# Optimization experiments

Measured on AMD Instinct MI355X. Metric: run time of the kernel, lower is better.

## Reference

```python
import jax, jax.numpy as jnp
import numpy as np

N_NODES = 100000
N_EDGES = 3200000
NUM_FEATURES = 256
NUM_CLASSES = 1000


def gcn_conv(x, edge_index, W, b):
    # PyG GCNConv: h = XW; add self-loops; out = D^{-1/2} (A+I) D^{-1/2} h + b
    n = x.shape[0]
    h = x @ W  # [N, out]
    loop = jnp.arange(n)
    src = jnp.concatenate([edge_index[0], loop])
    dst = jnp.concatenate([edge_index[1], loop])
    ones = jnp.ones(src.shape[0], dtype=x.dtype)
    deg = jax.ops.segment_sum(ones, dst, num_segments=n)  # in-degree incl. self-loop
    dinv = jax.lax.rsqrt(deg)  # deg >= 1 because of self-loops
    norm = dinv[src] * dinv[dst]  # [E+N]
    out = jax.ops.segment_sum(h[src] * norm[:, None], dst, num_segments=n)
    return out + b


def setup_inputs() -> dict:
    key = jax.random.key(0)
    ks = jax.random.split(key, 12)
    x = jax.random.normal(ks[0], (N_NODES, NUM_FEATURES), dtype=jnp.float32)
    edge_index = jax.random.randint(ks[1], (2, N_EDGES), 0, N_NODES, dtype=jnp.int64)
    def glorot(k, shape):
        fan_in, fan_out = shape[0], shape[-1]
        lim = np.sqrt(6.0 / (fan_in + fan_out)).astype(np.float32)
        return jax.random.uniform(k, shape, jnp.float32, -lim, lim)
    W1 = glorot(ks[2], (NUM_FEATURES, 16)); b1 = jnp.zeros((16,), jnp.float32)
    W2 = glorot(ks[3], (16, 32));           b2 = jnp.zeros((32,), jnp.float32)
    conv_w = jax.random.normal(ks[4], (64, 32, 1, 3), jnp.float32) * 0.05  # OIHW
    conv_b = jnp.zeros((64,), jnp.float32)
    fc_w = jax.random.normal(ks[5], (NUM_CLASSES, 64), jnp.float32) * 0.05
    fc_b = jnp.zeros((NUM_CLASSES,), jnp.float32)
    return {"x": x, "edge_index": edge_index, "W1": W1, "b1": b1,
            "W2": W2, "b2": b2, "conv_w": conv_w, "conv_b": conv_b,
            "fc_w": fc_w, "fc_b": fc_b}


def reference(x, edge_index, W1, b1, W2, b2, conv_w, conv_b, fc_w, fc_b):
    h = jax.nn.relu(gcn_conv(x, edge_index, W1, b1))   # [N,16]
    h = gcn_conv(h, edge_index, W2, b2)                 # [N,32]
    # x.unsqueeze(0).transpose(1,2) -> [1, 32, N]; run Conv2d((1,3), pad (0,1))
    # as NCHW with H=1: [1, 32, 1, N]
    img = h.T[None, :, None, :]                         # [1,32,1,N]
    y = jax.lax.conv_general_dilated(
        img, conv_w, window_strides=(1, 1), padding=((0, 0), (1, 1)),
        dimension_numbers=("NCHW", "OIHW", "NCHW"))
    y = y + conv_b[None, :, None, None]                 # [1,64,1,N]
    # adaptive_max_pool2d to (1,1) == global max over spatial dims
    pooled = jnp.max(y, axis=(2, 3))                    # [1,64]
    return pooled @ fc_w.T + fc_b                       # [1,num_classes]
```

## Files before the change

### kernel.cpp

```cpp
#include <hip/hip_runtime.h>
#include <hip/hip_bf16.h>
#include <hip/hip_fp16.h>

#define NN 100000
#define NE 3200000
#define FIN 256
#define F1 16
#define F2 32
#define CO 64
#define NC 1000
#define NBLK 391
#define GBLK 1563
#define NPART 8
#define NGRP 32
#define CAPG 16384
#define PSZ 12500
#define BK 20
#define SRCMASK 0x1FFFFu

#define OFF_DINV 0
#define OFF_CUR  100352
#define OFF_DEG  200704
#define OFF_ECOL 301056
#define OFF_MISC 3501056
#define OFF_EPART 3502080
#define OFF_HIST  7696384
#define OFF_H1S   3502080
#define OFF_H2S   4302080
#define OFF_OUT2  5902080

__device__ __forceinline__ unsigned enc_f(float f) {
    unsigned u = __float_as_uint(f);
    return (u & 0x80000000u) ? ~u : (u | 0x80000000u);
}
__device__ __forceinline__ float dec_f(unsigned u) {
    return (u & 0x80000000u) ? __uint_as_float(u & 0x7fffffffu) : __uint_as_float(~u);
}

__global__ void k_init(unsigned* __restrict__ pcur, unsigned* __restrict__ pool) {
    int t = threadIdx.x;
    pcur[t] = (unsigned)t * CAPG;
    if (t < 64) pool[t] = 0u;
}

__global__ __launch_bounds__(256) void k_bucket(const int* __restrict__ ei,
                                                unsigned* __restrict__ pcur,
                                                unsigned* __restrict__ epart) {
    __shared__ unsigned wcnt[4][8];
    __shared__ unsigned woff[4][8];
    int t = threadIdx.x, lane = t & 63, w = t >> 6;
    int g = blockIdx.x & (NGRP - 1);
    int base = blockIdx.x * (256 * BK) + t;
    int dst[BK], src[BK];
    #pragma unroll
    for (int k = 0; k < BK; ++k) {
        dst[k] = ei[NE + base + k * 256];
        src[k] = ei[base + k * 256];
    }
    unsigned long long lt = (lane == 63) ? 0x7fffffffffffffffull
                                         : ((1ull << lane) - 1ull);
    unsigned cnt = 0;
    #pragma unroll
    for (int k = 0; k < BK; ++k) {
        int bin = (unsigned)dst[k] / PSZ;
        #pragma unroll
        for (int b = 0; b < 8; ++b) {
            unsigned long long m = __ballot(bin == b);
            if (lane == b) cnt += (unsigned)__popcll(m);
        }
    }
    if (lane < 8) wcnt[w][lane] = cnt;
    __syncthreads();
    if (t < 8) {
        unsigned c0 = wcnt[0][t], c1 = wcnt[1][t], c2 = wcnt[2][t], c3 = wcnt[3][t];
        unsigned b = atomicAdd(&pcur[t * NGRP + g], c0 + c1 + c2 + c3);
        woff[0][t] = b;
        woff[1][t] = b + c0;
        woff[2][t] = b + c0 + c1;
        woff[3][t] = b + c0 + c1 + c2;
    }
    __syncthreads();
    unsigned run = (lane < 8) ? woff[w][lane] : 0u;
    #pragma unroll
    for (int k = 0; k < BK; ++k) {
        int bin = (unsigned)dst[k] / PSZ;
        unsigned long long mym = 0;
        unsigned myrun = 0;
        #pragma unroll
        for (int b = 0; b < 8; ++b) {
            unsigned long long m = __ballot(bin == b);
            unsigned r = __shfl(run, b);
            if (bin == b) { mym = m; myrun = r; }
            if (lane == b) run += (unsigned)__popcll(m);
        }
        unsigned pos = myrun + (unsigned)__popcll(mym & lt);
        epart[pos] = ((unsigned)(dst[k] - bin * PSZ) << 17) | (unsigned)src[k];
    }
}

__global__ __launch_bounds__(256) void k_hist(const unsigned* __restrict__ pcur,
                                              const unsigned* __restrict__ epart,
                                              unsigned* __restrict__ hist) {
    __shared__ unsigned lh[PSZ];
    int p = blockIdx.x & 7;
    int g = blockIdx.x >> 3;
    int ci = p * NGRP + g;
    int t = threadIdx.x;
    for (int i = t; i < PSZ; i += 256) lh[i] = 0;
    __syncthreads();
    unsigned s = (unsigned)ci * CAPG;
    unsigned e = pcur[ci];
    for (unsigned j = s + t; j < e; j += 256)
        atomicAdd(&lh[epart[j] >> 17], 1u);
    __syncthreads();
    unsigned* hrow = hist + (unsigned)ci * PSZ;
    for (int i = t; i < PSZ; i += 256) hrow[i] = lh[i];
}

__global__ __launch_bounds__(256) void k_colscan(unsigned* __restrict__ hist,
                                                 unsigned* __restrict__ deg,
                                                 unsigned* __restrict__ bsum) {
    __shared__ unsigned W[4];
    int t = threadIdx.x;
    int gid = blockIdx.x * 256 + t;
    unsigned run = 0;
    if (gid < NN) {
        int p = gid / PSZ, i = gid % PSZ;
        #pragma unroll
        for (int c = 0; c < NGRP; ++c) {
            unsigned idx = (unsigned)(p * NGRP + c) * PSZ + i;
            unsigned v = hist[idx];
            hist[idx] = run;
            run += v;
        }
        deg[gid] = run;
    }
    unsigned d = (gid < NN) ? run : 0u;
    #pragma unroll
    for (int off = 1; off < 64; off <<= 1) d += __shfl_xor(d, off);
    if ((t & 63) == 0) W[t >> 6] = d;
    __syncthreads();
    if (t == 0) bsum[blockIdx.x] = W[0] + W[1] + W[2] + W[3];
}

__global__ __launch_bounds__(512) void k_bscan(unsigned* __restrict__ bsum) {
    __shared__ unsigned S[512];
    int t = threadIdx.x;
    unsigned v = (t < NBLK) ? bsum[t] : 0u;
    S[t] = v;
    __syncthreads();
    for (int off = 1; off < 512; off <<= 1) {
        unsigned u = (t >= off) ? S[t - off] : 0u;
        __syncthreads();
        S[t] += u;
        __syncthreads();
    }
    if (t < NBLK) bsum[t] = S[t] - v;
}

__global__ void k_cscan(const unsigned* __restrict__ deg, const unsigned* __restrict__ bsum,
                        unsigned* __restrict__ cursor, float* __restrict__ dinv) {
    __shared__ unsigned S[256];
    int t = threadIdx.x;
    int i = blockIdx.x * 256 + t;
    unsigned d = (i < NN) ? deg[i] : 0u;
    S[t] = d;
    __syncthreads();
    for (int off = 1; off < 256; off <<= 1) {
        unsigned u = (t >= off) ? S[t - off] : 0u;
        __syncthreads();
        S[t] += u;
        __syncthreads();
    }
    if (i < NN) {
        cursor[i] = bsum[blockIdx.x] + S[t];
        dinv[i] = rsqrtf((float)(d + 1u));
    }
}

__global__ __launch_bounds__(256) void k_place(const unsigned* __restrict__ pcur,
                                               const unsigned* __restrict__ epart,
                                               const unsigned* __restrict__ hist,
                                               const unsigned* __restrict__ cursor,
                                               int* __restrict__ ecol) {
    __shared__ unsigned lcur[PSZ];
    int p = blockIdx.x & 7;
    int g = blockIdx.x >> 3;
    int ci = p * NGRP + g;
    int t = threadIdx.x;
    int pb = p * PSZ;
    const unsigned* hrow = hist + (unsigned)ci * PSZ;
    for (int i = t; i < PSZ; i += 256) {
        int gi = pb + i;
        unsigned rowstart = gi ? cursor[gi - 1] : 0u;
        lcur[i] = rowstart + hrow[i];
    }
    __syncthreads();
    unsigned s = (unsigned)ci * CAPG;
    unsigned e = pcur[ci];
    for (unsigned j = s + t; j < e; j += 256) {
        unsigned v = epart[j];
        unsigned pos = atomicAdd(&lcur[v >> 17], 1u);
        ecol[pos] = (int)(v & SRCMASK);
    }
}

__device__ __forceinline__ void fma16g(float xk, const float* __restrict__ w,
                                       float* __restrict__ acc) {
    #pragma unroll
    for (int o = 0; o < 16; ++o) acc[o] += xk * w[o];
}

__global__ __launch_bounds__(64) void k_gemm1(const float* __restrict__ X,
                                              const float* __restrict__ W1,
                                              const float* __restrict__ dinv,
                                              __half2* __restrict__ h1h) {
    int row = blockIdx.x * 64 + threadIdx.x;
    if (row >= NN) return;
    const float4* xr = (const float4*)(X + (size_t)row * FIN);
    float acc[16] = {};
    #pragma unroll 1
    for (int c = 0; c < 8; ++c) {
        float4 xq[8];
        #pragma unroll
        for (int i = 0; i < 8; ++i) xq[i] = xr[c * 8 + i];
        const float* xf = (const float*)xq;
        #pragma unroll
        for (int kk = 0; kk < 32; ++kk)
            fma16g(xf[kk], W1 + (c * 32 + kk) * 16, acc);
    }
    float dv = dinv[row];
    union { __half2 h[8]; uint4 u[2]; } pk;
    #pragma unroll
    for (int o = 0; o < 8; ++o)
        pk.h[o] = __floats2half2_rn(acc[2 * o] * dv, acc[2 * o + 1] * dv);
    uint4* dst = (uint4*)(h1h + (size_t)row * 8);
    dst[0] = pk.u[0];
    dst[1] = pk.u[1];
}

__global__ __launch_bounds__(256) void k_gathm(const unsigned* __restrict__ cursor,
                                               const int* __restrict__ ecol,
                                               const float* __restrict__ dinv,
                                               const float* __restrict__ b1,
                                               const float* __restrict__ W2,
                                               const __half2* __restrict__ h1h,
                                               __half2* __restrict__ h2h) {
    __shared__ float Ws[512];
    __shared__ float B1[16];
    int tid = threadIdx.x;
    Ws[tid] = W2[tid];
    Ws[tid + 256] = W2[tid + 256];
    if (tid < 16) B1[tid] = b1[tid];
    __syncthreads();
    int lane = tid & 63;
    int grp = lane >> 3, f2 = lane & 7;
    int node = blockIdx.x * 32 + (tid >> 6) * 8 + grp;
    unsigned s = node ? cursor[node - 1] : 0u;
    unsigned e = cursor[node];
    float2 acc = __half22float2(h1h[(size_t)node * 8 + f2]);
    for (unsigned j = s; j < e; j += 8) {
        int cc[8]; float msk[8];
        #pragma unroll
        for (int q = 0; q < 8; ++q) {
            unsigned jj = j + q;
            bool v = jj < e;
            cc[q] = ecol[v ? jj : j];
            msk[q] = v ? 1.f : 0.f;
        }
        float2 a[8];
        #pragma unroll
        for (int q = 0; q < 8; ++q)
            a[q] = __half22float2(h1h[(size_t)cc[q] * 8 + f2]);
        #pragma unroll
        for (int q = 0; q < 8; ++q) {
            acc.x += msk[q] * a[q].x;
            acc.y += msk[q] * a[q].y;
        }
    }
    float dv = dinv[node];
    float r0 = fmaxf(acc.x * dv + B1[2 * f2], 0.f);
    float r1 = fmaxf(acc.y * dv + B1[2 * f2 + 1], 0.f);
    int gb = lane & 56;
    float rv[16];
    #pragma unroll
    for (int q = 0; q < 8; ++q) {
        rv[2 * q]     = __shfl(r0, gb + q);
        rv[2 * q + 1] = __shfl(r1, gb + q);
    }
    float o0x = 0.f, o0y = 0.f, o1x = 0.f, o1y = 0.f;
    #pragma unroll
    for (int q = 0; q < 16; ++q) {
        float r = rv[q];
        o0x += r * Ws[q * 32 + 2 * f2];
        o0y += r * Ws[q * 32 + 2 * f2 + 1];
        o1x += r * Ws[q * 32 + 2 * f2 + 16];
        o1y += r * Ws[q * 32 + 2 * f2 + 17];
    }
    h2h[(size_t)node * 16 + f2]     = __floats2half2_rn(o0x * dv, o0y * dv);
    h2h[(size_t)node * 16 + f2 + 8] = __floats2half2_rn(o1x * dv, o1y * dv);
}

__global__ __launch_bounds__(256) void k_gath2(const unsigned* __restrict__ cursor,
                                               const int* __restrict__ ecol,
                                               const float* __restrict__ dinv,
                                               const float* __restrict__ b2,
                                               const __half2* __restrict__ h2h,
                                               float* __restrict__ out2) {
    int tid = threadIdx.x;
    int lane = tid & 63;
    int grp = lane >> 4, f2 = lane & 15;
    int node = blockIdx.x * 16 + (tid >> 6) * 4 + grp;
    unsigned s = node ? cursor[node - 1] : 0u;
    unsigned e = cursor[node];
    float2 acc = __half22float2(h2h[(size_t)node * 16 + f2]);
    for (unsigned j = s; j < e; j += 8) {
        int cc[8]; float msk[8];
        #pragma unroll
        for (int q = 0; q < 8; ++q) {
            unsigned jj = j + q;
            bool v = jj < e;
            cc[q] = ecol[v ? jj : j];
            msk[q] = v ? 1.f : 0.f;
        }
        float2 a[8];
        #pragma unroll
        for (int q = 0; q < 8; ++q)
            a[q] = __half22float2(h2h[(size_t)cc[q] * 16 + f2]);
        #pragma unroll
        for (int q = 0; q < 8; ++q) {
            acc.x += msk[q] * a[q].x;
            acc.y += msk[q] * a[q].y;
        }
    }
    float dv = dinv[node];
    float2 b = ((const float2*)b2)[f2];
    ((float2*)(out2 + (size_t)node * F2))[f2] =
        make_float2(acc.x * dv + b.x, acc.y * dv + b.y);
}

#define NPB 256
__global__ __launch_bounds__(256) void k_conv(const float* __restrict__ h2f,
                                              const float* __restrict__ cw,
                                              unsigned* __restrict__ pool) {
    __shared__ float Hs[NPB + 2][33];
    __shared__ float Wt[3 * 32 * 64];
    __shared__ float4 Ms[4][16];
    int tid = threadIdx.x;
    int base = blockIdx.x * NPB;
    for (int idx = tid; idx < 6144; idx += 256) {
        int o = idx / 96, r = idx % 96, ci = r / 3, k = r % 3;
        Wt[(k * 32 + ci) * 64 + o] = cw[idx];
    }
    for (int idx = tid; idx < (NPB + 2) * 8; idx += 256) {
        int j = idx >> 3, c4 = (idx & 7) << 2;
        int g = base + j - 1;
        float4 v = make_float4(0.f, 0.f, 0.f, 0.f);
        if (g >= 0 && g < NN) v = *(const float4*)(h2f + (size_t)g * F2 + c4);
        Hs[j][c4 + 0] = v.x;
        Hs[j][c4 + 1] = v.y;
        Hs[j][c4 + 2] = v.z;
        Hs[j][c4 + 3] = v.w;
    }
    __syncthreads();

    int o4 = (tid & 15) * 4;
    int ng = tid >> 4;
    float4 acc[16] = {};
    for (int ci = 0; ci < 32; ++ci) {
        float h[18];
        #pragma unroll
        for (int j = 0; j < 18; ++j) h[j] = Hs[ng * 16 + j][ci];
        #pragma unroll
        for (int k = 0; k < 3; ++k) {
            float4 w = *(const float4*)&Wt[(k * 32 + ci) * 64 + o4];
            #pragma unroll
            for (int i = 0; i < 16; ++i) {
                float hv = h[i + k];
                acc[i].x += hv * w.x;
                acc[i].y += hv * w.y;
                acc[i].z += hv * w.z;
                acc[i].w += hv * w.w;
            }
        }
    }
    const float NI = -3.0e38f;
    float4 m4 = make_float4(NI, NI, NI, NI);
    #pragma unroll
    for (int i = 0; i < 16; ++i) {
        if (base + ng * 16 + i < NN) {
            m4.x = fmaxf(m4.x, acc[i].x);
            m4.y = fmaxf(m4.y, acc[i].y);
            m4.z = fmaxf(m4.z, acc[i].z);
            m4.w = fmaxf(m4.w, acc[i].w);
        }
    }
    #pragma unroll
    for (int off = 16; off <= 32; off <<= 1) {
        m4.x = fmaxf(m4.x, __shfl_xor(m4.x, off));
        m4.y = fmaxf(m4.y, __shfl_xor(m4.y, off));
        m4.z = fmaxf(m4.z, __shfl_xor(m4.z, off));
        m4.w = fmaxf(m4.w, __shfl_xor(m4.w, off));
    }
    int lane = tid & 63, wv = tid >> 6;
    if (lane < 16) Ms[wv][lane] = m4;
    __syncthreads();
    if (tid < 16) {
        float4 a = Ms[0][tid], b = Ms[1][tid], c = Ms[2][tid], d = Ms[3][tid];
        a.x = fmaxf(fmaxf(a.x, b.x), fmaxf(c.x, d.x));
        a.y = fmaxf(fmaxf(a.y, b.y), fmaxf(c.y, d.y));
        a.z = fmaxf(fmaxf(a.z, b.z), fmaxf(c.z, d.z));
        a.w = fmaxf(fmaxf(a.w, b.w), fmaxf(c.w, d.w));
        int o = tid * 4;
        atomicMax(&pool[o + 0], enc_f(a.x));
        atomicMax(&pool[o + 1], enc_f(a.y));
        atomicMax(&pool[o + 2], enc_f(a.z));
        atomicMax(&pool[o + 3], enc_f(a.w));
    }
}

__global__ void k_fc(const unsigned* __restrict__ pool, const float* __restrict__ cb,
                     const float* __restrict__ fw, const float* __restrict__ fb,
                     float* __restrict__ out) {
    __shared__ float P[64];
    int tid = threadIdx.x;
    if (tid < 64) P[tid] = dec_f(pool[tid]) + cb[tid];
    __syncthreads();
    int j = blockIdx.x * 256 + tid;
    if (j >= NC) return;
    float s = fb[j];
    const float4* wr = (const float4*)(fw + (size_t)j * CO);
    #pragma unroll
    for (int c = 0; c < 16; ++c) {
        float4 w = wr[c];
        s += P[c * 4 + 0] * w.x + P[c * 4 + 1] * w.y +
             P[c * 4 + 2] * w.z + P[c * 4 + 3] * w.w;
    }
    out[j] = s;
}

extern "C" void kernel_launch(void* const* d_in, const int* in_sizes, int n_in,
                              void* d_out, int out_size, void* d_ws, size_t ws_size,
                              hipStream_t stream) {
    const float* x  = (const float*)d_in[0];
    const int*   ei = (const int*)d_in[1];
    const float* W1 = (const float*)d_in[2];
    const float* b1 = (const float*)d_in[3];
    const float* W2 = (const float*)d_in[4];
    const float* b2 = (const float*)d_in[5];
    const float* cw = (const float*)d_in[6];
    const float* cb = (const float*)d_in[7];
    const float* fw = (const float*)d_in[8];
    const float* fb = (const float*)d_in[9];

    float* ws = (float*)d_ws;
    float*    dinv   = ws + OFF_DINV;
    unsigned* cursor = (unsigned*)(ws + OFF_CUR);
    unsigned* deg    = (unsigned*)(ws + OFF_DEG);
    int*      ecol   = (int*)(ws + OFF_ECOL);
    unsigned* pcur   = (unsigned*)(ws + OFF_MISC);
    unsigned* pool   = pcur + 256;
    unsigned* bsum   = pcur + 320;
    unsigned* epart  = (unsigned*)(ws + OFF_EPART);
    unsigned* hist   = (unsigned*)(ws + OFF_HIST);
    __half2*  h1h    = (__half2*)(ws + OFF_H1S);
    __half2*  h2h    = (__half2*)(ws + OFF_H2S);
    float*    out2   = ws + OFF_OUT2;

    k_init   <<<1, 256, 0, stream>>>(pcur, pool);
    k_bucket <<<NE / (256 * BK), 256, 0, stream>>>(ei, pcur, epart);
    k_hist   <<<NPART * NGRP, 256, 0, stream>>>(pcur, epart, hist);
    k_colscan<<<NBLK, 256, 0, stream>>>(hist, deg, bsum);
    k_bscan  <<<1, 512, 0, stream>>>(bsum);
    k_cscan  <<<NBLK, 256, 0, stream>>>(deg, bsum, cursor, dinv);
    k_place  <<<NPART * NGRP, 256, 0, stream>>>(pcur, epart, hist, cursor, ecol);
    k_gemm1  <<<GBLK, 64, 0, stream>>>(x, W1, dinv, h1h);
    k_gathm  <<<NN / 32, 256, 0, stream>>>(cursor, ecol, dinv, b1, W2, h1h, h2h);
    k_gath2  <<<NN / 16, 256, 0, stream>>>(cursor, ecol, dinv, b2, h2h, out2);
    k_conv   <<<(NN + NPB - 1) / NPB, 256, 0, stream>>>(out2, cw, pool);
    k_fc     <<<4, 256, 0, stream>>>(pool, cb, fw, fb, (float*)d_out);
}
```

Before: 245.2 us.

## Load edge indices cooperatively via shuffles and store layer-2 output as fp16

In both gather kernels each lane now loads one edge column index and broadcasts it to its feature group with shuffles, instead of every lane redundantly loading all indices. k_gath2 also processes 16 edges per iteration. The layer-2 output is stored as half2 rather than float, and the conv kernel unpacks it back to float in shared memory. This cuts redundant index loads and halves the intermediate write/read traffic, at the cost of extra shuffle instructions and fp16 rounding of the conv input.

```diff
diff --git a/kernel.cpp b/kernel.cpp
--- a/kernel.cpp
+++ b/kernel.cpp
@@ -27,7 +27,7 @@
 #define OFF_HIST  7696384
 #define OFF_H1S   3502080
 #define OFF_H2S   4302080
-#define OFF_OUT2  5902080
+#define OFF_OUT2H 5902080
 
 __device__ __forceinline__ unsigned enc_f(float f) {
     unsigned u = __float_as_uint(f);
@@ -255,33 +255,31 @@
     __syncthreads();
     int lane = tid & 63;
     int grp = lane >> 3, f2 = lane & 7;
+    int gb = lane & 56;
     int node = blockIdx.x * 32 + (tid >> 6) * 8 + grp;
     unsigned s = node ? cursor[node - 1] : 0u;
     unsigned e = cursor[node];
     float2 acc = __half22float2(h1h[(size_t)node * 8 + f2]);
     for (unsigned j = s; j < e; j += 8) {
-        int cc[8]; float msk[8];
+        unsigned jj = j + (unsigned)f2;
+        int myc = ecol[jj < e ? jj : j];
+        int cq[8];
+        #pragma unroll
+        for (int q = 0; q < 8; ++q) cq[q] = __shfl(myc, gb + q);
+        float2 a[8];
+        #pragma unroll
+        for (int q = 0; q < 8; ++q)
+            a[q] = __half22float2(h1h[(size_t)cq[q] * 8 + f2]);
         #pragma unroll
         for (int q = 0; q < 8; ++q) {
-            unsigned jj = j + q;
-            bool v = jj < e;
-            cc[q] = ecol[v ? jj : j];
-            msk[q] = v ? 1.f : 0.f;
-        }
-        float2 a[8];
-        #pragma unroll
-        for (int q = 0; q < 8; ++q)
-            a[q] = __half22float2(h1h[(size_t)cc[q] * 8 + f2]);
-        #pragma unroll
-        for (int q = 0; q < 8; ++q) {
-            acc.x += msk[q] * a[q].x;
-            acc.y += msk[q] * a[q].y;
+            float m = (j + q < e) ? 1.f : 0.f;
+            acc.x += m * a[q].x;
+            acc.y += m * a[q].y;
         }
     }
     float dv = dinv[node];
     float r0 = fmaxf(acc.x * dv + B1[2 * f2], 0.f);
     float r1 = fmaxf(acc.y * dv + B1[2 * f2 + 1], 0.f);
-    int gb = lane & 56;
     float rv[16];
     #pragma unroll
     for (int q = 0; q < 8; ++q) {
@@ -306,41 +304,40 @@
                                                const float* __restrict__ dinv,
                                                const float* __restrict__ b2,
                                                const __half2* __restrict__ h2h,
-                                               float* __restrict__ out2) {
+                                               __half2* __restrict__ out2h) {
     int tid = threadIdx.x;
     int lane = tid & 63;
     int grp = lane >> 4, f2 = lane & 15;
+    int gb = lane & 48;
     int node = blockIdx.x * 16 + (tid >> 6) * 4 + grp;
     unsigned s = node ? cursor[node - 1] : 0u;
     unsigned e = cursor[node];
     float2 acc = __half22float2(h2h[(size_t)node * 16 + f2]);
-    for (unsigned j = s; j < e; j += 8) {
-        int cc[8]; float msk[8];
-        #pragma unroll
-        for (int q = 0; q < 8; ++q) {
-            unsigned jj = j + q;
-            bool v = jj < e;
-            cc[q] = ecol[v ? jj : j];
-            msk[q] = v ? 1.f : 0.f;
-        }
-        float2 a[8];
-        #pragma unroll
-        for (int q = 0; q < 8; ++q)
-            a[q] = __half22float2(h2h[(size_t)cc[q] * 16 + f2]);
-        #pragma unroll
-        for (int q = 0; q < 8; ++q) {
-            acc.x += msk[q] * a[q].x;
-            acc.y += msk[q] * a[q].y;
+    for (unsigned j = s; j < e; j += 16) {
+        unsigned jj = j + (unsigned)f2;
+        int myc = ecol[jj < e ? jj : j];
+        int cq[16];
+        #pragma unroll
+        for (int q = 0; q < 16; ++q) cq[q] = __shfl(myc, gb + q);
+        float2 a[16];
+        #pragma unroll
+        for (int q = 0; q < 16; ++q)
+            a[q] = __half22float2(h2h[(size_t)cq[q] * 16 + f2]);
+        #pragma unroll
+        for (int q = 0; q < 16; ++q) {
+            float m = (j + q < e) ? 1.f : 0.f;
+            acc.x += m * a[q].x;
+            acc.y += m * a[q].y;
         }
     }
     float dv = dinv[node];
     float2 b = ((const float2*)b2)[f2];
-    ((float2*)(out2 + (size_t)node * F2))[f2] =
-        make_float2(acc.x * dv + b.x, acc.y * dv + b.y);
+    out2h[(size_t)node * 16 + f2] =
+        __floats2half2_rn(acc.x * dv + b.x, acc.y * dv + b.y);
 }
 
 #define NPB 256
-__global__ __launch_bounds__(256) void k_conv(const float* __restrict__ h2f,
+__global__ __launch_bounds__(256) void k_conv(const __half2* __restrict__ h2f,
                                               const float* __restrict__ cw,
                                               unsigned* __restrict__ pool) {
     __shared__ float Hs[NPB + 2][33];
@@ -352,15 +349,22 @@
         int o = idx / 96, r = idx % 96, ci = r / 3, k = r % 3;
         Wt[(k * 32 + ci) * 64 + o] = cw[idx];
     }
-    for (int idx = tid; idx < (NPB + 2) * 8; idx += 256) {
-        int j = idx >> 3, c4 = (idx & 7) << 2;
+    for (int idx = tid; idx < (NPB + 2) * 4; idx += 256) {
+        int j = idx >> 2, qt = idx & 3;
         int g = base + j - 1;
-        float4 v = make_float4(0.f, 0.f, 0.f, 0.f);
-        if (g >= 0 && g < NN) v = *(const float4*)(h2f + (size_t)g * F2 + c4);
-        Hs[j][c4 + 0] = v.x;
-        Hs[j][c4 + 1] = v.y;
-        Hs[j][c4 + 2] = v.z;
-        Hs[j][c4 + 3] = v.w;
+        if (g >= 0 && g < NN) {
+            uint4 v = *(const uint4*)(h2f + (size_t)g * 16 + qt * 4);
+            const __half2* hp = (const __half2*)&v;
+            #pragma unroll
+            for (int q = 0; q < 4; ++q) {
+                float2 f = __half22float2(hp[q]);
+                Hs[j][qt * 8 + 2 * q]     = f.x;
+                Hs[j][qt * 8 + 2 * q + 1] = f.y;
+            }
+        } else {
+            #pragma unroll
+            for (int q = 0; q < 8; ++q) Hs[j][qt * 8 + q] = 0.f;
+        }
     }
     __syncthreads();
 
@@ -465,7 +469,7 @@
     unsigned* hist   = (unsigned*)(ws + OFF_HIST);
     __half2*  h1h    = (__half2*)(ws + OFF_H1S);
     __half2*  h2h    = (__half2*)(ws + OFF_H2S);
-    float*    out2   = ws + OFF_OUT2;
+    __half2*  out2h  = (__half2*)(ws + OFF_OUT2H);
 
     k_init   <<<1, 256, 0, stream>>>(pcur, pool);
     k_bucket <<<NE / (256 * BK), 256, 0, stream>>>(ei, pcur, epart);
@@ -476,7 +480,7 @@
     k_place  <<<NPART * NGRP, 256, 0, stream>>>(pcur, epart, hist, cursor, ecol);
     k_gemm1  <<<GBLK, 64, 0, stream>>>(x, W1, dinv, h1h);
     k_gathm  <<<NN / 32, 256, 0, stream>>>(cursor, ecol, dinv, b1, W2, h1h, h2h);
-    k_gath2  <<<NN / 16, 256, 0, stream>>>(cursor, ecol, dinv, b2, h2h, out2);
-    k_conv   <<<(NN + NPB - 1) / NPB, 256, 0, stream>>>(out2, cw, pool);
+    k_gath2  <<<NN / 16, 256, 0, stream>>>(cursor, ecol, dinv, b2, h2h, out2h);
+    k_conv   <<<(NN + NPB - 1) / NPB, 256, 0, stream>>>(out2h, cw, pool);
     k_fc     <<<4, 256, 0, stream>>>(pool, cb, fw, fb, (float*)d_out);
 }
```

Result: no change. 241.9 us (-1.3%).
